# Performance work log

Hardware: AMD Instinct MI355X
Metric: run time of the kernel (lower is better)

Reference implementation:

```python
import jax, jax.numpy as jnp
import numpy as np

B, S, D, H, E = 8192, 256, 32, 256, 32
START_TOK = 2


def setup_inputs() -> dict:
    key = jax.random.key(0)
    ks = jax.random.split(key, 12)
    sc = 0.05  # small init so LSTM/logits stay numerically tame
    n = lambda k, sh: (jax.random.normal(k, sh, dtype=jnp.float32) * sc)
    return {
        "states": jax.random.normal(ks[0], (B, S), dtype=jnp.float32),
        "actions": jax.random.randint(ks[1], (B, D), 0, 2, dtype=jnp.int64).astype(jnp.int32),
        "se_W": n(ks[2], (H, S)),
        "se_b": jnp.zeros((H,), jnp.float32),
        "aemb": n(ks[3], (START_TOK + 1, E)),
        "W_ih0": n(ks[4], (4 * H, H + E)),
        "W_hh0": n(ks[5], (4 * H, H)),
        "b_ih0": jnp.zeros((4 * H,), jnp.float32),
        "b_hh0": jnp.zeros((4 * H,), jnp.float32),
        "W_ih1": n(ks[6], (4 * H, H)),
        "W_hh1": n(ks[7], (4 * H, H)),
        "b_ih1": jnp.zeros((4 * H,), jnp.float32),
        "b_hh1": jnp.zeros((4 * H,), jnp.float32),
        "heads_W": n(ks[8], (D, H, 2)),
        "heads_b": jnp.zeros((D, 2), jnp.float32),
    }


def _lstm_cell(x, h, c, Wih, Whh, bih, bhh):
    # PyTorch gate order: input, forget, cell(g), output
    g = x @ Wih.T + h @ Whh.T + bih + bhh  # [B, 4H]
    i, f, gg, o = jnp.split(g, 4, axis=-1)
    i, f, o = jax.nn.sigmoid(i), jax.nn.sigmoid(f), jax.nn.sigmoid(o)
    cn = f * c + i * jnp.tanh(gg)
    return o * jnp.tanh(cn), cn


def reference(states, actions, se_W, se_b, aemb,
              W_ih0, W_hh0, b_ih0, b_hh0, W_ih1, W_hh1, b_ih1, b_hh1,
              heads_W, heads_b):
    Bm = states.shape[0]
    s_emb = jax.nn.relu(states @ se_W.T + se_b)            # [B, H]
    prev0 = jnp.broadcast_to(aemb[START_TOK], (Bm, E))     # start-token embedding
    zeros_h = jnp.zeros((Bm, H), states.dtype)
    carry0 = (zeros_h, zeros_h, zeros_h, zeros_h, prev0,
              jnp.zeros((Bm,), states.dtype), jnp.zeros((Bm,), states.dtype))

    def step(carry, x):
        h0, c0, h1, c1, prev, tlp, tent = carry
        a_i, hW, hb = x                                    # [B], [H,2], [2]
        inp = jnp.concatenate([s_emb, prev], axis=-1)      # [B, H+E]
        h0n, c0n = _lstm_cell(inp, h0, c0, W_ih0, W_hh0, b_ih0, b_hh0)
        h1n, c1n = _lstm_cell(h0n, h1, c1, W_ih1, W_hh1, b_ih1, b_hh1)
        logits = h1n @ hW + hb                             # [B, 2]
        logp = jax.nn.log_softmax(logits, axis=-1)
        lp_i = jnp.take_along_axis(logp, a_i[:, None], axis=1)[:, 0]
        ent_i = -jnp.sum(jnp.exp(logp) * logp, axis=-1)
        prev_n = aemb[a_i]                                 # [B, E]
        new_carry = (h0n, c0n, h1n, c1n, prev_n, tlp + lp_i, tent + ent_i)
        return new_carry, (tlp, ent_i)                     # prefix lp BEFORE adding

    xs = (actions.T, heads_W, heads_b)                     # leading axis = D steps
    (h0, c0, h1, c1, prev, tot_lp, tot_ent), (prefix, per_ent) = jax.lax.scan(step, carry0, xs)
    prefix_lps = prefix.T                                  # [B, D]
    per_ent = jax.lax.stop_gradient(per_ent.T)             # detached in original
    return tot_lp, tot_ent, prefix_lps, per_ent
```

## Files before the change

kernel.cpp:

```cpp
#include <hip/hip_runtime.h>
#include <hip/hip_bf16.h>

#define B_ 8192
#define S_ 256
#define D_ 32
#define H_ 256
#define E_ 32
#define BT 32
#define NTH 512

typedef short bf16x8 __attribute__((ext_vector_type(8)));
typedef float f32x4 __attribute__((ext_vector_type(4)));

__device__ __forceinline__ unsigned short f2bf(float x) {
  __hip_bfloat16 h = __float2bfloat16(x);
  return *reinterpret_cast<unsigned short*>(&h);
}
__device__ __forceinline__ float bf2f(unsigned short u) {
  __hip_bfloat16 h = *reinterpret_cast<__hip_bfloat16*>(&u);
  return __bfloat162float(h);
}
__device__ __forceinline__ float sigf_(float x) { return 1.f / (1.f + __expf(-x)); }
__device__ __forceinline__ float tanhf_(float x) {
  float e = __expf(-2.f * fabsf(x));
  float r = (1.f - e) / (1.f + e);
  return copysignf(r, x);
}


__global__ void packB_k(const float* __restrict__ src, unsigned short* __restrict__ dst,
                        int N, int srcStride, int srcOff) {
  int g = blockIdx.x * blockDim.x + threadIdx.x;
  int total = N * 256 / 8;
  if (g >= total) return;
  int lane = g & 63, kt = (g >> 6) & 7, nt = g >> 9;
  int n = nt * 16 + (lane & 15);
  int k = kt * 32 + (lane >> 4) * 8;
  const float* s = src + (size_t)n * srcStride + srcOff + k;
#pragma unroll
  for (int e = 0; e < 8; ++e) dst[(size_t)g * 8 + e] = f2bf(s[e]);
}

__global__ void ptab_k(const float* __restrict__ aemb, const float* __restrict__ Wih0,
                       float* __restrict__ ptab) {
  int n = blockIdx.x * blockDim.x + threadIdx.x;
  if (n >= 1024) return;
  for (int tok = 0; tok < 3; ++tok) {
    float acc = 0.f;
    for (int e = 0; e < E_; ++e)
      acc = fmaf(aemb[tok * E_ + e], Wih0[(size_t)n * 288 + 256 + e], acc);
    ptab[tok * 1024 + n] = acc;
  }
}

__global__ void actmask_k(const int* __restrict__ a, unsigned* __restrict__ m) {
  int b = blockIdx.x * blockDim.x + threadIdx.x;
  if (b >= B_) return;
  unsigned v = 0;
  for (int t = 0; t < D_; ++t) v |= (unsigned)(a[(size_t)b * D_ + t] & 1) << t;
  m[b] = v;
}


__device__ __forceinline__ int haddr(int row, int colbyte) {
  return (row * 512 + colbyte) ^ ((row & 7) << 4);
}

template <int NG>
__device__ __forceinline__ void gemm_frag(f32x4 acc[2][2][NG], const unsigned short* __restrict__ Wp,
                                          const char* __restrict__ Abuf, int lane, int ntBase,
                                          int ntStride) {
  const int l15 = lane & 15, l4 = lane >> 4;
#pragma unroll
  for (int kt = 0; kt < 8; ++kt) {
    bf16x8 a[2];
#pragma unroll
    for (int m = 0; m < 2; ++m) {
      int row = m * 16 + l15;
      a[m] = *(const bf16x8*)(Abuf + haddr(row, kt * 64 + l4 * 16));
    }
#pragma unroll
    for (int g = 0; g < NG; ++g) {
#pragma unroll
      for (int js = 0; js < 2; ++js) {
        int nt = ntBase + g * ntStride + js;
        bf16x8 b = *(const bf16x8*)(Wp + (((size_t)nt * 8 + kt) * 64 + lane) * 8);
#pragma unroll
        for (int m = 0; m < 2; ++m)
          acc[m][js][g] = __builtin_amdgcn_mfma_f32_16x16x32_bf16(a[m], b, acc[m][js][g], 0, 0, 0);
      }
    }
  }
}

__global__ __launch_bounds__(NTH, 2)
void actor_main(const float* __restrict__ states,
                const unsigned short* __restrict__ seWP,
                const float* __restrict__ se_b,
                const unsigned short* __restrict__ W0sP,
                const float* __restrict__ b_ih0, const float* __restrict__ b_hh0,
                const unsigned short* __restrict__ Whh0P,
                const unsigned short* __restrict__ Wih1P,
                const unsigned short* __restrict__ Whh1P,
                const float* __restrict__ b_ih1, const float* __restrict__ b_hh1,
                const float* __restrict__ ptabw,
                const unsigned* __restrict__ amaskw,
                const float* __restrict__ headsW,
                const float* __restrict__ headsb,
                float* __restrict__ out) {
  __shared__ char stA[16384];
  __shared__ char h0s[16384];
  __shared__ char h1s[16384];
  __shared__ unsigned amask_s[BT];

  const int tid = threadIdx.x;
  const int lane = tid & 63, wave = tid >> 6;
  const int l15 = lane & 15, l4 = lane >> 4;
  const int b0 = blockIdx.x * BT;
  const int wj = wave * 32;

  {
    int row = tid >> 4, c0i = (tid & 15) * 16;
    const float* sp = states + (size_t)(b0 + row) * S_ + c0i;
    union { unsigned short us[8]; int4 v; } ck0, ck1;
#pragma unroll
    for (int e = 0; e < 8; ++e) ck0.us[e] = f2bf(sp[e]);
#pragma unroll
    for (int e = 0; e < 8; ++e) ck1.us[e] = f2bf(sp[8 + e]);
    *(int4*)(stA + haddr(row, c0i * 2)) = ck0.v;
    *(int4*)(stA + haddr(row, c0i * 2 + 16)) = ck1.v;
  }
  if (tid < BT) amask_s[tid] = amaskw[b0 + tid];
  __syncthreads();

  {
    f32x4 acc2[2][2][1];
#pragma unroll
    for (int m = 0; m < 2; ++m)
#pragma unroll
      for (int js = 0; js < 2; ++js) acc2[m][js][0] = (f32x4){0.f, 0.f, 0.f, 0.f};
    gemm_frag<1>(acc2, seWP, stA, lane, wave * 2, 0);
    float seb[2] = {se_b[wj + l15], se_b[wj + 16 + l15]};
#pragma unroll
    for (int m = 0; m < 2; ++m)
#pragma unroll
      for (int js = 0; js < 2; ++js)
#pragma unroll
        for (int r = 0; r < 4; ++r) {
          float v = fmaxf(acc2[m][js][0][r] + seb[js], 0.f);
          int row = m * 16 + l4 * 4 + r, col = wj + js * 16 + l15;
          *(unsigned short*)(h1s + haddr(row, col * 2)) = f2bf(v);
        }
  }
  __syncthreads();

  f32x4 x0r[2][2][4];
  {
    float bias[2][4];
#pragma unroll
    for (int js = 0; js < 2; ++js)
#pragma unroll
      for (int g = 0; g < 4; ++g) {
        int n = g * 256 + wj + js * 16 + l15;
        bias[js][g] = b_ih0[n] + b_hh0[n];
      }
#pragma unroll
    for (int m = 0; m < 2; ++m)
#pragma unroll
      for (int js = 0; js < 2; ++js)
#pragma unroll
        for (int g = 0; g < 4; ++g) {
          float bb = bias[js][g];
          x0r[m][js][g] = (f32x4){bb, bb, bb, bb};
        }
    gemm_frag<4>(x0r, W0sP, h1s, lane, wave * 2, 16);
  }
  __syncthreads();

  for (int i = tid; i < 1024; i += NTH) {
    ((int4*)h0s)[i] = make_int4(0, 0, 0, 0);
    ((int4*)h1s)[i] = make_int4(0, 0, 0, 0);
  }
  __syncthreads();

  float pt[3][2][4], b1b[2][4];
#pragma unroll
  for (int js = 0; js < 2; ++js)
#pragma unroll
    for (int g = 0; g < 4; ++g) {
      int n = g * 256 + wj + js * 16 + l15;
      pt[0][js][g] = ptabw[n];
      pt[1][js][g] = ptabw[1024 + n];
      pt[2][js][g] = ptabw[2048 + n];
      b1b[js][g] = b_ih1[n] + b_hh1[n];
    }
  unsigned am[2][4];
#pragma unroll
  for (int m = 0; m < 2; ++m)
#pragma unroll
    for (int r = 0; r < 4; ++r) am[m][r] = amask_s[m * 16 + l4 * 4 + r];

  float c0v[2][2][4], c1v[2][2][4];
#pragma unroll
  for (int m = 0; m < 2; ++m)
#pragma unroll
    for (int js = 0; js < 2; ++js)
#pragma unroll
      for (int r = 0; r < 4; ++r) { c0v[m][js][r] = 0.f; c1v[m][js][r] = 0.f; }

  const int hrow = wave * 4 + l4;
  const unsigned hmask = amask_s[hrow];
  float tlp = 0.f, tent = 0.f;

#pragma unroll 1
  for (int t = 0; t < D_; ++t) {
    f32x4 acc[2][2][4];
#pragma unroll
    for (int m = 0; m < 2; ++m)
#pragma unroll
      for (int js = 0; js < 2; ++js)
#pragma unroll
        for (int g = 0; g < 4; ++g)
#pragma unroll
          for (int r = 0; r < 4; ++r) {
            float p;
            if (t == 0) p = pt[2][js][g];
            else p = ((am[m][r] >> (t - 1)) & 1) ? pt[1][js][g] : pt[0][js][g];
            acc[m][js][g][r] = x0r[m][js][g][r] + p;
          }
    gemm_frag<4>(acc, Whh0P, h0s, lane, wave * 2, 16);

    unsigned short hn[2][2][4];
#pragma unroll
    for (int m = 0; m < 2; ++m)
#pragma unroll
      for (int js = 0; js < 2; ++js)
#pragma unroll
        for (int r = 0; r < 4; ++r) {
          float ig = sigf_(acc[m][js][0][r]);
          float fg = sigf_(acc[m][js][1][r]);
          float gg = tanhf_(acc[m][js][2][r]);
          float og = sigf_(acc[m][js][3][r]);
          float c = fg * c0v[m][js][r] + ig * gg;
          c0v[m][js][r] = c;
          hn[m][js][r] = f2bf(og * tanhf_(c));
        }
    __syncthreads();
#pragma unroll
    for (int m = 0; m < 2; ++m)
#pragma unroll
      for (int js = 0; js < 2; ++js)
#pragma unroll
        for (int r = 0; r < 4; ++r) {
          int row = m * 16 + l4 * 4 + r, col = wj + js * 16 + l15;
          *(unsigned short*)(h0s + haddr(row, col * 2)) = hn[m][js][r];
        }
    __syncthreads();

#pragma unroll
    for (int m = 0; m < 2; ++m)
#pragma unroll
      for (int js = 0; js < 2; ++js)
#pragma unroll
        for (int g = 0; g < 4; ++g) {
          float bb = b1b[js][g];
          acc[m][js][g] = (f32x4){bb, bb, bb, bb};
        }
    gemm_frag<4>(acc, Wih1P, h0s, lane, wave * 2, 16);
    gemm_frag<4>(acc, Whh1P, h1s, lane, wave * 2, 16);

#pragma unroll
    for (int m = 0; m < 2; ++m)
#pragma unroll
      for (int js = 0; js < 2; ++js)
#pragma unroll
        for (int r = 0; r < 4; ++r) {
          float ig = sigf_(acc[m][js][0][r]);
          float fg = sigf_(acc[m][js][1][r]);
          float gg = tanhf_(acc[m][js][2][r]);
          float og = sigf_(acc[m][js][3][r]);
          float c = fg * c1v[m][js][r] + ig * gg;
          c1v[m][js][r] = c;
          hn[m][js][r] = f2bf(og * tanhf_(c));
        }
    __syncthreads();
#pragma unroll
    for (int m = 0; m < 2; ++m)
#pragma unroll
      for (int js = 0; js < 2; ++js)
#pragma unroll
        for (int r = 0; r < 4; ++r) {
          int row = m * 16 + l4 * 4 + r, col = wj + js * 16 + l15;
          *(unsigned short*)(h1s + haddr(row, col * 2)) = hn[m][js][r];
        }
    __syncthreads();

    float p0 = 0.f, p1 = 0.f;
    const float* hw = headsW + (size_t)t * 512;
#pragma unroll
    for (int jj = 0; jj < 16; ++jj) {
      int j = l15 + jj * 16;
      float h = bf2f(*(const unsigned short*)(h1s + haddr(hrow, j * 2)));
      float2 w = *(const float2*)(hw + j * 2);
      p0 = fmaf(h, w.x, p0);
      p1 = fmaf(h, w.y, p1);
    }
#pragma unroll
    for (int mm = 1; mm < 16; mm <<= 1) {
      p0 += __shfl_xor(p0, mm, 64);
      p1 += __shfl_xor(p1, mm, 64);
    }
    float l0 = p0 + headsb[t * 2 + 0], l1 = p1 + headsb[t * 2 + 1];
    float mx = fmaxf(l0, l1);
    float e0 = __expf(l0 - mx), e1 = __expf(l1 - mx);
    float Z = e0 + e1;
    float lse = mx + __logf(Z);
    float lp0 = l0 - lse, lp1 = l1 - lse;
    float ent = -(e0 * lp0 + e1 * lp1) / Z;
    int a = (hmask >> t) & 1;
    float lp = a ? lp1 : lp0;
    if (l15 == 0) {
      int rowg = b0 + hrow;
      out[2 * B_ + (size_t)rowg * D_ + t] = tlp;
      out[2 * B_ + B_ * D_ + (size_t)rowg * D_ + t] = ent;
    }
    tlp += lp;
    tent += ent;
  }
  if (l15 == 0) {
    int rowg = b0 + hrow;
    out[rowg] = tlp;
    out[B_ + rowg] = tent;
  }
}


extern "C" void kernel_launch(void* const* d_in, const int* in_sizes, int n_in,
                              void* d_out, int out_size, void* d_ws, size_t ws_size,
                              hipStream_t stream) {
  const float* states = (const float*)d_in[0];
  const int* actions = (const int*)d_in[1];
  const float* se_W = (const float*)d_in[2];
  const float* se_b = (const float*)d_in[3];
  const float* aemb = (const float*)d_in[4];
  const float* W_ih0 = (const float*)d_in[5];
  const float* W_hh0 = (const float*)d_in[6];
  const float* b_ih0 = (const float*)d_in[7];
  const float* b_hh0 = (const float*)d_in[8];
  const float* W_ih1 = (const float*)d_in[9];
  const float* W_hh1 = (const float*)d_in[10];
  const float* b_ih1 = (const float*)d_in[11];
  const float* b_hh1 = (const float*)d_in[12];
  const float* headsW = (const float*)d_in[13];
  const float* headsb = (const float*)d_in[14];
  float* out = (float*)d_out;
  char* ws = (char*)d_ws;

  unsigned short* seWP  = (unsigned short*)(ws + 0);
  unsigned short* W0sP  = (unsigned short*)(ws + 131072);
  unsigned short* Whh0P = (unsigned short*)(ws + 655360);
  unsigned short* Wih1P = (unsigned short*)(ws + 1179648);
  unsigned short* Whh1P = (unsigned short*)(ws + 1703936);
  float* ptabw          = (float*)(ws + 2228224);
  unsigned* amaskw      = (unsigned*)(ws + 2240512);

  hipLaunchKernelGGL(packB_k, dim3(32), dim3(256), 0, stream, se_W, seWP, 256, 256, 0);
  hipLaunchKernelGGL(packB_k, dim3(128), dim3(256), 0, stream, W_ih0, W0sP, 1024, 288, 0);
  hipLaunchKernelGGL(packB_k, dim3(128), dim3(256), 0, stream, W_hh0, Whh0P, 1024, 256, 0);
  hipLaunchKernelGGL(packB_k, dim3(128), dim3(256), 0, stream, W_ih1, Wih1P, 1024, 256, 0);
  hipLaunchKernelGGL(packB_k, dim3(128), dim3(256), 0, stream, W_hh1, Whh1P, 1024, 256, 0);
  hipLaunchKernelGGL(ptab_k, dim3(4), dim3(256), 0, stream, aemb, W_ih0, ptabw);
  hipLaunchKernelGGL(actmask_k, dim3(32), dim3(256), 0, stream, actions, amaskw);
  hipLaunchKernelGGL(actor_main, dim3(B_ / BT), dim3(NTH), 0, stream,
                     states, seWP, se_b, W0sP, b_ih0, b_hh0, Whh0P, Wih1P, Whh1P,
                     b_ih1, b_hh1, ptabw, amaskw, headsW, headsb, out);
}
```

Before: 4.624 ms.

## Split LSTM gate columns across 16 waves and pack precomputed inputs as bf16

Doubles the block to 1024 threads, so each wave owns 16 hidden columns across the four gates instead of 32. Weight fragments are addressed by a per-lane base pointer, and the head reduction is spread over 32 lanes per row. This aims to raise in-block parallelism and latency hiding on the serial recurrence. The precomputed input projections, token table and biases are held as packed bf16 to cut register pressure, at some precision cost. It also means more waves taking part in each barrier and more LDS A-fragment reads per MFMA.

New measurement: 3.924 ms. -15.1%, faster.

```diff
diff --git a/kernel.cpp b/kernel.cpp
--- a/kernel.cpp
+++ b/kernel.cpp
@@ -7,7 +7,7 @@
 #define H_ 256
 #define E_ 32
 #define BT 32
-#define NTH 512
+#define NTH 1024
 
 typedef short bf16x8 __attribute__((ext_vector_type(8)));
 typedef float f32x4 __attribute__((ext_vector_type(4)));
@@ -16,9 +16,13 @@
   __hip_bfloat16 h = __float2bfloat16(x);
   return *reinterpret_cast<unsigned short*>(&h);
 }
+__device__ __forceinline__ unsigned pack2bf(float a, float b) {
+  return (unsigned)f2bf(a) | ((unsigned)f2bf(b) << 16);
+}
+__device__ __forceinline__ float lo_bf(unsigned u) { return __uint_as_float(u << 16); }
+__device__ __forceinline__ float hi_bf(unsigned u) { return __uint_as_float(u & 0xffff0000u); }
 __device__ __forceinline__ float bf2f(unsigned short u) {
-  __hip_bfloat16 h = *reinterpret_cast<__hip_bfloat16*>(&u);
-  return __bfloat162float(h);
+  return __uint_as_float((unsigned)u << 16);
 }
 __device__ __forceinline__ float sigf_(float x) { return 1.f / (1.f + __expf(-x)); }
 __device__ __forceinline__ float tanhf_(float x) {
@@ -67,33 +71,22 @@
 }
 
 template <int NG>
-__device__ __forceinline__ void gemm_frag(f32x4 acc[2][2][NG], const unsigned short* __restrict__ Wp,
-                                          const char* __restrict__ Abuf, int lane, int ntBase,
-                                          int ntStride) {
-  const int l15 = lane & 15, l4 = lane >> 4;
+__device__ __forceinline__ void gemm_frag(f32x4 acc[2][NG], const unsigned short* __restrict__ Wlane,
+                                          const char* __restrict__ Abuf, int l15, int l4) {
 #pragma unroll
   for (int kt = 0; kt < 8; ++kt) {
-    bf16x8 a[2];
-#pragma unroll
-    for (int m = 0; m < 2; ++m) {
-      int row = m * 16 + l15;
-      a[m] = *(const bf16x8*)(Abuf + haddr(row, kt * 64 + l4 * 16));
-    }
+    bf16x8 a0 = *(const bf16x8*)(Abuf + haddr(l15, kt * 64 + l4 * 16));
+    bf16x8 a1 = *(const bf16x8*)(Abuf + haddr(16 + l15, kt * 64 + l4 * 16));
 #pragma unroll
     for (int g = 0; g < NG; ++g) {
-#pragma unroll
-      for (int js = 0; js < 2; ++js) {
-        int nt = ntBase + g * ntStride + js;
-        bf16x8 b = *(const bf16x8*)(Wp + (((size_t)nt * 8 + kt) * 64 + lane) * 8);
-#pragma unroll
-        for (int m = 0; m < 2; ++m)
-          acc[m][js][g] = __builtin_amdgcn_mfma_f32_16x16x32_bf16(a[m], b, acc[m][js][g], 0, 0, 0);
-      }
-    }
-  }
-}
-
-__global__ __launch_bounds__(NTH, 2)
+      bf16x8 b = *(const bf16x8*)(Wlane + g * 65536 + kt * 512);
+      acc[0][g] = __builtin_amdgcn_mfma_f32_16x16x32_bf16(a0, b, acc[0][g], 0, 0, 0);
+      acc[1][g] = __builtin_amdgcn_mfma_f32_16x16x32_bf16(a1, b, acc[1][g], 0, 0, 0);
+    }
+  }
+}
+
+__global__ __launch_bounds__(NTH)
 void actor_main(const float* __restrict__ states,
                 const unsigned short* __restrict__ seWP,
                 const float* __restrict__ se_b,
@@ -117,9 +110,9 @@
   const int lane = tid & 63, wave = tid >> 6;
   const int l15 = lane & 15, l4 = lane >> 4;
   const int b0 = blockIdx.x * BT;
-  const int wj = wave * 32;
-
-  {
+  const int wbase = wave * 4096 + lane * 8;
+
+  if (tid < 512) {
     int row = tid >> 4, c0i = (tid & 15) * 16;
     const float* sp = states + (size_t)(b0 + row) * S_ + c0i;
     union { unsigned short us[8]; int4 v; } ck0, ck1;
@@ -134,179 +127,169 @@
   __syncthreads();
 
   {
-    f32x4 acc2[2][2][1];
-#pragma unroll
-    for (int m = 0; m < 2; ++m)
-#pragma unroll
-      for (int js = 0; js < 2; ++js) acc2[m][js][0] = (f32x4){0.f, 0.f, 0.f, 0.f};
-    gemm_frag<1>(acc2, seWP, stA, lane, wave * 2, 0);
-    float seb[2] = {se_b[wj + l15], se_b[wj + 16 + l15]};
-#pragma unroll
-    for (int m = 0; m < 2; ++m)
-#pragma unroll
-      for (int js = 0; js < 2; ++js)
-#pragma unroll
-        for (int r = 0; r < 4; ++r) {
-          float v = fmaxf(acc2[m][js][0][r] + seb[js], 0.f);
-          int row = m * 16 + l4 * 4 + r, col = wj + js * 16 + l15;
-          *(unsigned short*)(h1s + haddr(row, col * 2)) = f2bf(v);
-        }
+    f32x4 a1[2][1];
+#pragma unroll
+    for (int m = 0; m < 2; ++m) a1[m][0] = (f32x4){0.f, 0.f, 0.f, 0.f};
+    gemm_frag<1>(a1, seWP + wbase, stA, l15, l4);
+    float seb = se_b[wave * 16 + l15];
+#pragma unroll
+    for (int m = 0; m < 2; ++m)
+#pragma unroll
+      for (int r = 0; r < 4; ++r) {
+        float v = fmaxf(a1[m][0][r] + seb, 0.f);
+        *(unsigned short*)(h1s + haddr(m * 16 + l4 * 4 + r, (wave * 16 + l15) * 2)) = f2bf(v);
+      }
   }
   __syncthreads();
 
-  f32x4 x0r[2][2][4];
+  unsigned x0p[2][4][2];
   {
-    float bias[2][4];
-#pragma unroll
-    for (int js = 0; js < 2; ++js)
-#pragma unroll
-      for (int g = 0; g < 4; ++g) {
-        int n = g * 256 + wj + js * 16 + l15;
-        bias[js][g] = b_ih0[n] + b_hh0[n];
-      }
-#pragma unroll
-    for (int m = 0; m < 2; ++m)
-#pragma unroll
-      for (int js = 0; js < 2; ++js)
-#pragma unroll
-        for (int g = 0; g < 4; ++g) {
-          float bb = bias[js][g];
-          x0r[m][js][g] = (f32x4){bb, bb, bb, bb};
-        }
-    gemm_frag<4>(x0r, W0sP, h1s, lane, wave * 2, 16);
+    f32x4 xa[2][4];
+#pragma unroll
+    for (int m = 0; m < 2; ++m)
+#pragma unroll
+      for (int g = 0; g < 4; ++g) xa[m][g] = (f32x4){0.f, 0.f, 0.f, 0.f};
+    gemm_frag<4>(xa, W0sP + wbase, h1s, l15, l4);
+#pragma unroll
+    for (int g = 0; g < 4; ++g) {
+      int n = g * 256 + wave * 16 + l15;
+      float bias = b_ih0[n] + b_hh0[n];
+#pragma unroll
+      for (int m = 0; m < 2; ++m) {
+        x0p[m][g][0] = pack2bf(xa[m][g][0] + bias, xa[m][g][1] + bias);
+        x0p[m][g][1] = pack2bf(xa[m][g][2] + bias, xa[m][g][3] + bias);
+      }
+    }
   }
   __syncthreads();
 
-  for (int i = tid; i < 1024; i += NTH) {
-    ((int4*)h0s)[i] = make_int4(0, 0, 0, 0);
-    ((int4*)h1s)[i] = make_int4(0, 0, 0, 0);
+  for (int i = tid; i < 2048; i += NTH) {
+    ((int4*)h0s)[i & 1023] = make_int4(0, 0, 0, 0);
+    if (i >= 1024) ((int4*)h1s)[i & 1023] = make_int4(0, 0, 0, 0);
   }
   __syncthreads();
 
-  float pt[3][2][4], b1b[2][4];
-#pragma unroll
-  for (int js = 0; js < 2; ++js)
-#pragma unroll
-    for (int g = 0; g < 4; ++g) {
-      int n = g * 256 + wj + js * 16 + l15;
-      pt[0][js][g] = ptabw[n];
-      pt[1][js][g] = ptabw[1024 + n];
-      pt[2][js][g] = ptabw[2048 + n];
-      b1b[js][g] = b_ih1[n] + b_hh1[n];
-    }
-  unsigned am[2][4];
+  unsigned ptp[3][2], b1p[2];
+#pragma unroll
+  for (int tok = 0; tok < 3; ++tok)
+#pragma unroll
+    for (int j = 0; j < 2; ++j) {
+      int n0 = (2 * j) * 256 + wave * 16 + l15, n1 = (2 * j + 1) * 256 + wave * 16 + l15;
+      ptp[tok][j] = pack2bf(ptabw[tok * 1024 + n0], ptabw[tok * 1024 + n1]);
+    }
+#pragma unroll
+  for (int j = 0; j < 2; ++j) {
+    int n0 = (2 * j) * 256 + wave * 16 + l15, n1 = (2 * j + 1) * 256 + wave * 16 + l15;
+    b1p[j] = pack2bf(b_ih1[n0] + b_hh1[n0], b_ih1[n1] + b_hh1[n1]);
+  }
+  float b1g[4] = {lo_bf(b1p[0]), hi_bf(b1p[0]), lo_bf(b1p[1]), hi_bf(b1p[1])};
+
+  float c0v[2][4], c1v[2][4];
 #pragma unroll
   for (int m = 0; m < 2; ++m)
 #pragma unroll
-    for (int r = 0; r < 4; ++r) am[m][r] = amask_s[m * 16 + l4 * 4 + r];
-
-  float c0v[2][2][4], c1v[2][2][4];
-#pragma unroll
-  for (int m = 0; m < 2; ++m)
-#pragma unroll
-    for (int js = 0; js < 2; ++js)
-#pragma unroll
-      for (int r = 0; r < 4; ++r) { c0v[m][js][r] = 0.f; c1v[m][js][r] = 0.f; }
-
-  const int hrow = wave * 4 + l4;
+    for (int r = 0; r < 4; ++r) { c0v[m][r] = 0.f; c1v[m][r] = 0.f; }
+
+  const int hrow = wave * 2 + (lane >> 5);
+  const int l31 = lane & 31;
   const unsigned hmask = amask_s[hrow];
   float tlp = 0.f, tent = 0.f;
 
 #pragma unroll 1
   for (int t = 0; t < D_; ++t) {
-    f32x4 acc[2][2][4];
-#pragma unroll
-    for (int m = 0; m < 2; ++m)
-#pragma unroll
-      for (int js = 0; js < 2; ++js)
-#pragma unroll
-        for (int g = 0; g < 4; ++g)
-#pragma unroll
-          for (int r = 0; r < 4; ++r) {
-            float p;
-            if (t == 0) p = pt[2][js][g];
-            else p = ((am[m][r] >> (t - 1)) & 1) ? pt[1][js][g] : pt[0][js][g];
-            acc[m][js][g][r] = x0r[m][js][g][r] + p;
-          }
-    gemm_frag<4>(acc, Whh0P, h0s, lane, wave * 2, 16);
-
-    unsigned short hn[2][2][4];
-#pragma unroll
-    for (int m = 0; m < 2; ++m)
-#pragma unroll
-      for (int js = 0; js < 2; ++js)
-#pragma unroll
-        for (int r = 0; r < 4; ++r) {
-          float ig = sigf_(acc[m][js][0][r]);
-          float fg = sigf_(acc[m][js][1][r]);
-          float gg = tanhf_(acc[m][js][2][r]);
-          float og = sigf_(acc[m][js][3][r]);
-          float c = fg * c0v[m][js][r] + ig * gg;
-          c0v[m][js][r] = c;
-          hn[m][js][r] = f2bf(og * tanhf_(c));
+    float p0g[4], p1g[4];
+    if (t == 0) {
+#pragma unroll
+      for (int j = 0; j < 2; ++j) {
+        p0g[2 * j] = lo_bf(ptp[2][j]); p0g[2 * j + 1] = hi_bf(ptp[2][j]);
+        p1g[2 * j] = p0g[2 * j];       p1g[2 * j + 1] = p0g[2 * j + 1];
+      }
+    } else {
+#pragma unroll
+      for (int j = 0; j < 2; ++j) {
+        p0g[2 * j] = lo_bf(ptp[0][j]); p0g[2 * j + 1] = hi_bf(ptp[0][j]);
+        p1g[2 * j] = lo_bf(ptp[1][j]); p1g[2 * j + 1] = hi_bf(ptp[1][j]);
+      }
+    }
+
+    f32x4 acc[2][4];
+#pragma unroll
+    for (int m = 0; m < 2; ++m)
+#pragma unroll
+      for (int r = 0; r < 4; ++r) {
+        unsigned msk = amask_s[m * 16 + l4 * 4 + r];
+        bool hi1 = t ? (((msk >> (t - 1)) & 1u) != 0u) : false;
+#pragma unroll
+        for (int g = 0; g < 4; ++g) {
+          float x0v = (r & 1) ? hi_bf(x0p[m][g][r >> 1]) : lo_bf(x0p[m][g][r >> 1]);
+          acc[m][g][r] = x0v + (hi1 ? p1g[g] : p0g[g]);
         }
+      }
+    gemm_frag<4>(acc, Whh0P + wbase, h0s, l15, l4);
+
+    unsigned short hn[2][4];
+#pragma unroll
+    for (int m = 0; m < 2; ++m)
+#pragma unroll
+      for (int r = 0; r < 4; ++r) {
+        float ig = sigf_(acc[m][0][r]);
+        float fg = sigf_(acc[m][1][r]);
+        float gg = tanhf_(acc[m][2][r]);
+        float og = sigf_(acc[m][3][r]);
+        float c = fg * c0v[m][r] + ig * gg;
+        c0v[m][r] = c;
+        hn[m][r] = f2bf(og * tanhf_(c));
+      }
     __syncthreads();
 #pragma unroll
     for (int m = 0; m < 2; ++m)
 #pragma unroll
-      for (int js = 0; js < 2; ++js)
-#pragma unroll
-        for (int r = 0; r < 4; ++r) {
-          int row = m * 16 + l4 * 4 + r, col = wj + js * 16 + l15;
-          *(unsigned short*)(h0s + haddr(row, col * 2)) = hn[m][js][r];
-        }
+      for (int r = 0; r < 4; ++r)
+        *(unsigned short*)(h0s + haddr(m * 16 + l4 * 4 + r, (wave * 16 + l15) * 2)) = hn[m][r];
     __syncthreads();
 
 #pragma unroll
     for (int m = 0; m < 2; ++m)
 #pragma unroll
-      for (int js = 0; js < 2; ++js)
-#pragma unroll
-        for (int g = 0; g < 4; ++g) {
-          float bb = b1b[js][g];
-          acc[m][js][g] = (f32x4){bb, bb, bb, bb};
-        }
-    gemm_frag<4>(acc, Wih1P, h0s, lane, wave * 2, 16);
-    gemm_frag<4>(acc, Whh1P, h1s, lane, wave * 2, 16);
-
-#pragma unroll
-    for (int m = 0; m < 2; ++m)
-#pragma unroll
-      for (int js = 0; js < 2; ++js)
-#pragma unroll
-        for (int r = 0; r < 4; ++r) {
-          float ig = sigf_(acc[m][js][0][r]);
-          float fg = sigf_(acc[m][js][1][r]);
-          float gg = tanhf_(acc[m][js][2][r]);
-          float og = sigf_(acc[m][js][3][r]);
-          float c = fg * c1v[m][js][r] + ig * gg;
-          c1v[m][js][r] = c;
-          hn[m][js][r] = f2bf(og * tanhf_(c));
-        }
+      for (int g = 0; g < 4; ++g) {
+        float bb = b1g[g];
+        acc[m][g] = (f32x4){bb, bb, bb, bb};
+      }
+    gemm_frag<4>(acc, Wih1P + wbase, h0s, l15, l4);
+    gemm_frag<4>(acc, Whh1P + wbase, h1s, l15, l4);
+
+#pragma unroll
+    for (int m = 0; m < 2; ++m)
+#pragma unroll
+      for (int r = 0; r < 4; ++r) {
+        float ig = sigf_(acc[m][0][r]);
+        float fg = sigf_(acc[m][1][r]);
+        float gg = tanhf_(acc[m][2][r]);
+        float og = sigf_(acc[m][3][r]);
+        float c = fg * c1v[m][r] + ig * gg;
+        c1v[m][r] = c;
+        hn[m][r] = f2bf(og * tanhf_(c));
+      }
     __syncthreads();
 #pragma unroll
     for (int m = 0; m < 2; ++m)
 #pragma unroll
-      for (int js = 0; js < 2; ++js)
-#pragma unroll
-        for (int r = 0; r < 4; ++r) {
-          int row = m * 16 + l4 * 4 + r, col = wj + js * 16 + l15;
-          *(unsigned short*)(h1s + haddr(row, col * 2)) = hn[m][js][r];
-        }
+      for (int r = 0; r < 4; ++r)
+        *(unsigned short*)(h1s + haddr(m * 16 + l4 * 4 + r, (wave * 16 + l15) * 2)) = hn[m][r];
     __syncthreads();
 
     float p0 = 0.f, p1 = 0.f;
     const float* hw = headsW + (size_t)t * 512;
 #pragma unroll
-    for (int jj = 0; jj < 16; ++jj) {
-      int j = l15 + jj * 16;
+    for (int jj = 0; jj < 8; ++jj) {
+      int j = l31 + jj * 32;
       float h = bf2f(*(const unsigned short*)(h1s + haddr(hrow, j * 2)));
       float2 w = *(const float2*)(hw + j * 2);
       p0 = fmaf(h, w.x, p0);
       p1 = fmaf(h, w.y, p1);
     }
 #pragma unroll
-    for (int mm = 1; mm < 16; mm <<= 1) {
+    for (int mm = 1; mm < 32; mm <<= 1) {
       p0 += __shfl_xor(p0, mm, 64);
       p1 += __shfl_xor(p1, mm, 64);
     }
@@ -319,7 +302,7 @@
     float ent = -(e0 * lp0 + e1 * lp1) / Z;
     int a = (hmask >> t) & 1;
     float lp = a ? lp1 : lp0;
-    if (l15 == 0) {
+    if (l31 == 0) {
       int rowg = b0 + hrow;
       out[2 * B_ + (size_t)rowg * D_ + t] = tlp;
       out[2 * B_ + B_ * D_ + (size_t)rowg * D_ + t] = ent;
@@ -327,7 +310,7 @@
     tlp += lp;
     tent += ent;
   }
-  if (l15 == 0) {
+  if (l31 == 0) {
     int rowg = b0 + hrow;
     out[rowg] = tlp;
     out[B_ + rowg] = tent;
```
